# Kernel optimization log

Measured on AMD Instinct MI355X. Metric: run time of the kernel, lower is better.

## Reference

```python
import jax, jax.numpy as jnp
import numpy as np

# dims
B, T = 64, 512
L = 3                 # number of HMLSTM layers
IN = 512              # per-layer input size (all equal)
D = L * IN            # 1536 total input size
E = 1024              # embedding_size
H1, H2 = 1024, 1024   # linear_sizes
O = 512               # output_size


def setup_inputs() -> dict:
    key = jax.random.key(0)
    ks = jax.random.split(key, 12)
    s = 0.02
    return {
        "x": jax.random.normal(ks[0], (B, T, D), dtype=jnp.float32),
        # gate linears: Linear(sum(input_sizes) -> 1, bias=False), one per layer, stacked [L, D]
        "Wg": jax.random.normal(ks[1], (L, D), dtype=jnp.float32) * s,
        # per-layer embedding linears Linear(IN -> E), stacked [L, E, IN] / [L, E]
        "We": jax.random.normal(ks[2], (L, E, IN), dtype=jnp.float32) * s,
        "be": jax.random.normal(ks[3], (L, E), dtype=jnp.float32) * s,
        # tanh MLP stack
        "W1": jax.random.normal(ks[4], (H1, E), dtype=jnp.float32) * s,
        "b1": jax.random.normal(ks[5], (H1,), dtype=jnp.float32) * s,
        "W2": jax.random.normal(ks[6], (H2, H1), dtype=jnp.float32) * s,
        "b2": jax.random.normal(ks[7], (H2,), dtype=jnp.float32) * s,
        # output head
        "Wo": jax.random.normal(ks[8], (O, H2), dtype=jnp.float32) * s,
        "bo": jax.random.normal(ks[9], (O,), dtype=jnp.float32) * s,
    }


def reference(x, Wg, We, be, W1, b1, W2, b2, Wo, bo):
    b, t, d = x.shape
    h = x.reshape(b * t, d)                       # per-timestep features, fully batched over time
    # gates: sigmoid(Linear(full h -> 1)) per layer -> [N, L]
    g = jax.nn.sigmoid(h @ Wg.T)
    # split full input into per-layer chunks (equal sizes -> reshape) and gate them
    hl = h.reshape(b * t, L, IN) * g[:, :, None]  # [N, L, IN]
    # s = sum_l Linear_l(h_l * g_l); biases sum since each embedding adds its own bias
    s = jnp.einsum("nli,lei->ne", hl, We) + be.sum(axis=0)
    he = jax.nn.relu(s)
    # fnn: tanh-activated linear stack
    o = jnp.tanh(he @ W1.T + b1)
    o = jnp.tanh(o @ W2.T + b2)
    out = o @ Wo.T + bo
    return out.reshape(b, t, O)
```

## Files before the change

kernel.cpp:

```cpp
#include <hip/hip_runtime.h>
#include <math.h>


typedef __attribute__((ext_vector_type(8))) short short8;
typedef __attribute__((ext_vector_type(4))) float float4v;

#define DEV __device__ __forceinline__

DEV unsigned short f2bf(float f){
    union{float f; unsigned int i;} c; c.f = f;
    unsigned int r = c.i + 0x7fffu + ((c.i>>16)&1u);
    return (unsigned short)(r>>16);
}
DEV unsigned int pack2(float a, float b){
    return (unsigned int)f2bf(a) | ((unsigned int)f2bf(b)<<16);
}

DEV void gload_lds16(const unsigned short* g, unsigned short* l){
    __builtin_amdgcn_global_load_lds((const __attribute__((address_space(1))) void*)g,
                                     (__attribute__((address_space(3))) void*)l, 16, 0, 0);
}

__global__ __launch_bounds__(256) void cvt_flat(const float* __restrict__ src,
                                                unsigned short* __restrict__ dst, int n8)
{
    int v = blockIdx.x*256 + threadIdx.x;
    if(v >= n8) return;
    const float4* s = (const float4*)(src) + v*2;
    float4 a = s[0], b = s[1];
    uint4 o;
    o.x = pack2(a.x, a.y); o.y = pack2(a.z, a.w);
    o.z = pack2(b.x, b.y); o.w = pack2(b.z, b.w);
    *((uint4*)dst + v) = o;
}

__global__ __launch_bounds__(256) void cvt_we(const float* __restrict__ We,
                                              unsigned short* __restrict__ Wep)
{
    int v  = blockIdx.x*256 + threadIdx.x;
    int i8 = v & 63;
    int e  = (v>>6) & 1023;
    int l  = v>>16;
    const float4* s = (const float4*)(We + (size_t)l*524288 + (size_t)e*512 + i8*8);
    float4 a = s[0], b = s[1];
    uint4 o;
    o.x = pack2(a.x, a.y); o.y = pack2(a.z, a.w);
    o.z = pack2(b.x, b.y); o.w = pack2(b.z, b.w);
    *(uint4*)(Wep + (size_t)e*1536 + (size_t)l*512 + i8*8) = o;
}

__global__ __launch_bounds__(256) void gate_u(const float* __restrict__ x,
                                              const float* __restrict__ Wg,
                                              unsigned short* __restrict__ u)
{
    int row  = blockIdx.x*4 + (threadIdx.x>>6);
    int lane = threadIdx.x & 63;
    const float4* xr = (const float4*)(x + (size_t)row*1536);
    float4 hv[6];
    #pragma unroll
    for(int j=0;j<6;j++) hv[j] = xr[j*64 + lane];

    float p[3];
    #pragma unroll
    for(int l=0;l<3;l++){
        const float4* wr = (const float4*)(Wg + (size_t)l*1536);
        float s = 0.f;
        #pragma unroll
        for(int j=0;j<6;j++){
            float4 wv = wr[j*64 + lane];
            s += hv[j].x*wv.x + hv[j].y*wv.y + hv[j].z*wv.z + hv[j].w*wv.w;
        }
        p[l] = s;
    }
    #pragma unroll
    for(int off=32; off; off>>=1){
        p[0] += __shfl_xor(p[0], off);
        p[1] += __shfl_xor(p[1], off);
        p[2] += __shfl_xor(p[2], off);
    }
    float g[3];
    #pragma unroll
    for(int l=0;l<3;l++) g[l] = 1.f/(1.f + __expf(-p[l]));

    uint2* ur = (uint2*)(u + (size_t)row*1536);
    #pragma unroll
    for(int j=0;j<6;j++){
        float gj = g[(j*64+lane)>>7];
        uint2 o;
        o.x = pack2(hv[j].x*gj, hv[j].y*gj);
        o.y = pack2(hv[j].z*gj, hv[j].w*gj);
        ur[j*64 + lane] = o;
    }
}

template<int ACT, int BIAS_ROWS, bool F32OUT>
__global__ __launch_bounds__(256) void gemm_bt(
    const unsigned short* __restrict__ A,
    const unsigned short* __restrict__ W,
    const float* __restrict__ bias,
    void* __restrict__ Cv,
    int M, int N, int K)
{
    __shared__ __align__(128) unsigned short As[128*32];
    __shared__ __align__(128) unsigned short Bs[128*32];

    int tid = threadIdx.x;
    int nb  = N >> 7;
    int bm  = blockIdx.x / nb;
    int bn  = blockIdx.x % nb;
    int m0  = bm << 7, n0 = bn << 7;
    int lane = tid & 63, wv = tid >> 6;
    int wm = wv >> 1, wn = wv & 1;
    int lr = lane & 15, quad = lane >> 4;

    float4v acc[4][4];
    #pragma unroll
    for(int i=0;i<4;i++)
        #pragma unroll
        for(int j=0;j<4;j++) acc[i][j] = (float4v){0.f,0.f,0.f,0.f};

    const unsigned short* gA = A + ((size_t)m0 + wv*32 + (lane>>2))*K + (lane&3)*8;
    const unsigned short* gB = W + ((size_t)n0 + wv*32 + (lane>>2))*K + (lane&3)*8;
    unsigned short* lA0 = &As[(wv*32)*32];
    unsigned short* lA1 = &As[(wv*32+16)*32];
    unsigned short* lB0 = &Bs[(wv*32)*32];
    unsigned short* lB1 = &Bs[(wv*32+16)*32];
    const size_t rstep = (size_t)16*K;

    for(int k0=0; k0<K; k0+=32){
        gload_lds16(gA,         lA0);
        gload_lds16(gA + rstep, lA1);
        gload_lds16(gB,         lB0);
        gload_lds16(gB + rstep, lB1);
        gA += 32; gB += 32;
        __syncthreads();

        short8 af[4], bfr[4];
        #pragma unroll
        for(int mi=0;mi<4;mi++)
            af[mi] = *(const short8*)(&As[(wm*64 + mi*16 + lr)*32 + quad*8]);
        #pragma unroll
        for(int ni=0;ni<4;ni++)
            bfr[ni] = *(const short8*)(&Bs[(wn*64 + ni*16 + lr)*32 + quad*8]);

        #pragma unroll
        for(int mi=0;mi<4;mi++)
            #pragma unroll
            for(int ni=0;ni<4;ni++)
                acc[mi][ni] = __builtin_amdgcn_mfma_f32_16x16x32_bf16(af[mi], bfr[ni], acc[mi][ni], 0, 0, 0);
        __syncthreads();
    }

    #pragma unroll
    for(int ni=0;ni<4;ni++){
        int n = n0 + wn*64 + ni*16 + lr;
        float bsum = 0.f;
        #pragma unroll
        for(int r=0;r<BIAS_ROWS;r++) bsum += bias[(size_t)r*N + n];
        #pragma unroll
        for(int mi=0;mi<4;mi++){
            #pragma unroll
            for(int reg=0;reg<4;reg++){
                int m = m0 + wm*64 + mi*16 + quad*4 + reg;
                float v = acc[mi][ni][reg] + bsum;
                if(ACT==1)      v = fmaxf(v, 0.f);
                else if(ACT==2) v = tanhf(v);
                if constexpr (F32OUT) ((float*)Cv)[(size_t)m*N + n] = v;
                else                  ((unsigned short*)Cv)[(size_t)m*N + n] = f2bf(v);
            }
        }
    }
}

extern "C" void kernel_launch(void* const* d_in, const int* in_sizes, int n_in,
                              void* d_out, int out_size, void* d_ws, size_t ws_size,
                              hipStream_t stream)
{
    const float* x  = (const float*)d_in[0];
    const float* Wg = (const float*)d_in[1];
    const float* We = (const float*)d_in[2];
    const float* be = (const float*)d_in[3];
    const float* W1 = (const float*)d_in[4];
    const float* b1 = (const float*)d_in[5];
    const float* W2 = (const float*)d_in[6];
    const float* b2 = (const float*)d_in[7];
    const float* Wo = (const float*)d_in[8];
    const float* bo = (const float*)d_in[9];
    float* out = (float*)d_out;

    const int M = 32768;

    char* w = (char*)d_ws;
    unsigned short* Wep   = (unsigned short*)w; w += (size_t)1024*1536*2;
    unsigned short* W1b   = (unsigned short*)w; w += (size_t)1024*1024*2;
    unsigned short* W2b   = (unsigned short*)w; w += (size_t)1024*1024*2;
    unsigned short* Wob   = (unsigned short*)w; w += (size_t)512*1024*2;
    unsigned short* slotA = (unsigned short*)w; w += (size_t)M*1536*2;
    unsigned short* slotB = (unsigned short*)w; w += (size_t)M*1024*2;
    unsigned short* u  = slotA;
    unsigned short* o1 = slotA;
    unsigned short* he = slotB;
    unsigned short* o2 = slotB;

    hipLaunchKernelGGL(cvt_flat, dim3(512), dim3(256), 0, stream, W1, W1b, 131072);
    hipLaunchKernelGGL(cvt_flat, dim3(512), dim3(256), 0, stream, W2, W2b, 131072);
    hipLaunchKernelGGL(cvt_flat, dim3(256), dim3(256), 0, stream, Wo, Wob, 65536);
    hipLaunchKernelGGL(cvt_we,   dim3(768), dim3(256), 0, stream, We, Wep);

    hipLaunchKernelGGL(gate_u, dim3(M/4), dim3(256), 0, stream, x, Wg, u);
    hipLaunchKernelGGL((gemm_bt<1,3,false>), dim3((M/128)*(1024/128)), dim3(256), 0, stream,
                       u,  Wep, be, he,  M, 1024, 1536);
    hipLaunchKernelGGL((gemm_bt<2,1,false>), dim3((M/128)*(1024/128)), dim3(256), 0, stream,
                       he, W1b, b1, o1,  M, 1024, 1024);
    hipLaunchKernelGGL((gemm_bt<2,1,false>), dim3((M/128)*(1024/128)), dim3(256), 0, stream,
                       o1, W2b, b2, o2,  M, 1024, 1024);
    hipLaunchKernelGGL((gemm_bt<0,1,true>),  dim3((M/128)*(512/128)),  dim3(256), 0, stream,
                       o2, Wob, bo, out, M, 512, 1024);
}
```

Before: 777.6 us.

## Double GEMM K-tile to 64 with XOR-swizzled LDS and XCD-aware block mapping

The GEMM K-step grows from 32 to 64, which halves the number of barrier pairs per tile. The LDS layout is XOR-swizzled per row so the 16-byte fragment reads avoid bank conflicts. Block indices are remapped so that each of the 8 XCDs processes a contiguous band of M tiles, which should improve L2 reuse of A rows. The cost is twice the shared memory per block, which may lower occupancy, and the remap assumes M/128 is divisible by 8.

```diff
diff --git a/kernel.cpp b/kernel.cpp
--- a/kernel.cpp
+++ b/kernel.cpp
@@ -101,14 +101,18 @@
     void* __restrict__ Cv,
     int M, int N, int K)
 {
-    __shared__ __align__(128) unsigned short As[128*32];
-    __shared__ __align__(128) unsigned short Bs[128*32];
+    __shared__ __align__(128) unsigned short As[128*64];
+    __shared__ __align__(128) unsigned short Bs[128*64];
 
     int tid = threadIdx.x;
     int nb  = N >> 7;
-    int bm  = blockIdx.x / nb;
-    int bn  = blockIdx.x % nb;
+    int mt  = M >> 7;
+    int xcd = blockIdx.x & 7;
+    int j   = blockIdx.x >> 3;
+    int bm  = xcd*(mt>>3) + j/nb;
+    int bn  = j % nb;
     int m0  = bm << 7, n0 = bn << 7;
+
     int lane = tid & 63, wv = tid >> 6;
     int wm = wv >> 1, wn = wv & 1;
     int lr = lane & 15, quad = lane >> 4;
@@ -117,37 +121,44 @@
     #pragma unroll
     for(int i=0;i<4;i++)
         #pragma unroll
-        for(int j=0;j<4;j++) acc[i][j] = (float4v){0.f,0.f,0.f,0.f};
-
-    const unsigned short* gA = A + ((size_t)m0 + wv*32 + (lane>>2))*K + (lane&3)*8;
-    const unsigned short* gB = W + ((size_t)n0 + wv*32 + (lane>>2))*K + (lane&3)*8;
-    unsigned short* lA0 = &As[(wv*32)*32];
-    unsigned short* lA1 = &As[(wv*32+16)*32];
-    unsigned short* lB0 = &Bs[(wv*32)*32];
-    unsigned short* lB1 = &Bs[(wv*32+16)*32];
-    const size_t rstep = (size_t)16*K;
-
-    for(int k0=0; k0<K; k0+=32){
-        gload_lds16(gA,         lA0);
-        gload_lds16(gA + rstep, lA1);
-        gload_lds16(gB,         lB0);
-        gload_lds16(gB + rstep, lB1);
-        gA += 32; gB += 32;
+        for(int jj=0;jj<4;jj++) acc[i][jj] = (float4v){0.f,0.f,0.f,0.f};
+
+    int rl  = lane >> 3;
+    int cbs = (lane & 7) ^ rl;
+    const unsigned short* gA = A + ((size_t)m0 + wv*32 + rl)*K + cbs*8;
+    const unsigned short* gB = W + ((size_t)n0 + wv*32 + rl)*K + cbs*8;
+    const size_t rstep = (size_t)8*K;
+
+    for(int k0=0; k0<K; k0+=64){
+        #pragma unroll
+        for(int d=0; d<4; d++){
+            gload_lds16(gA + d*rstep, &As[(wv*32 + d*8)*64]);
+            gload_lds16(gB + d*rstep, &Bs[(wv*32 + d*8)*64]);
+        }
+        gA += 64; gB += 64;
         __syncthreads();
 
-        short8 af[4], bfr[4];
-        #pragma unroll
-        for(int mi=0;mi<4;mi++)
-            af[mi] = *(const short8*)(&As[(wm*64 + mi*16 + lr)*32 + quad*8]);
-        #pragma unroll
-        for(int ni=0;ni<4;ni++)
-            bfr[ni] = *(const short8*)(&Bs[(wn*64 + ni*16 + lr)*32 + quad*8]);
-
-        #pragma unroll
-        for(int mi=0;mi<4;mi++)
-            #pragma unroll
-            for(int ni=0;ni<4;ni++)
-                acc[mi][ni] = __builtin_amdgcn_mfma_f32_16x16x32_bf16(af[mi], bfr[ni], acc[mi][ni], 0, 0, 0);
+        #pragma unroll
+        for(int ks=0; ks<2; ks++){
+            short8 af[4], bfr[4];
+            #pragma unroll
+            for(int mi=0;mi<4;mi++){
+                int row = wm*64 + mi*16 + lr;
+                int cbx = (ks*4 + quad) ^ (lr & 7);
+                af[mi] = *(const short8*)(&As[row*64 + cbx*8]);
+            }
+            #pragma unroll
+            for(int ni=0;ni<4;ni++){
+                int row = wn*64 + ni*16 + lr;
+                int cbx = (ks*4 + quad) ^ (lr & 7);
+                bfr[ni] = *(const short8*)(&Bs[row*64 + cbx*8]);
+            }
+            #pragma unroll
+            for(int mi=0;mi<4;mi++)
+                #pragma unroll
+                for(int ni=0;ni<4;ni++)
+                    acc[mi][ni] = __builtin_amdgcn_mfma_f32_16x16x32_bf16(af[mi], bfr[ni], acc[mi][ni], 0, 0, 0);
+        }
         __syncthreads();
     }
 
```

After: 733.4 us. 5.7% less time.
